# Optimization experiments

Measured on AMD Instinct MI355X. Metric: run time of the kernel, lower is better.

## Reference

```python
import jax, jax.numpy as jnp
import numpy as np

N, E, H = 20000, 320000, 5
IND, OUT = 64, 64
D2 = 2 * OUT          # 128
CAT = OUT + D2        # 192
BN_EPS = 1e-5


def _bn(x, g, b, m, v):
    # eval-mode BatchNorm1d
    return (x - m) * jax.lax.rsqrt(v + BN_EPS) * g + b


def _gcn(x, W, b, src, dst, n):
    # PyG GCNConv: add self-loops (already in src/dst), sym-normalized aggregation
    h = x @ W                                             # [N, C]
    deg = jax.ops.segment_sum(jnp.ones_like(dst, dtype=h.dtype), dst, num_segments=n)
    dinv = jnp.where(deg > 0, jax.lax.rsqrt(deg), 0.0)
    norm = dinv[src] * dinv[dst]                          # [E']
    out = jax.ops.segment_sum(h[src] * norm[:, None], dst, num_segments=n)
    return out + b


def _gat(x, W, att_src, att_dst, b, src, dst, n, heads, c):
    # PyG GATConv (concat=False): per-edge attention, segment softmax over dst
    hx = (x @ W).reshape(n, heads, c)                     # [N, H, C]
    a_s = jnp.einsum('nhc,hc->nh', hx, att_src)           # [N, H]
    a_d = jnp.einsum('nhc,hc->nh', hx, att_dst)
    e = jax.nn.leaky_relu(a_s[src] + a_d[dst], 0.2)       # [E', H]
    m = jax.ops.segment_max(e, dst, num_segments=n)       # every node has a self-loop
    w = jnp.exp(e - m[dst])
    den = jax.ops.segment_sum(w, dst, num_segments=n)
    alpha = w / den[dst]                                  # [E', H]
    out = jax.ops.segment_sum(hx[src] * alpha[:, :, None], dst, num_segments=n)  # [N,H,C]
    return out.mean(axis=1) + b


def setup_inputs() -> dict:
    key = jax.random.key(0)
    ks = iter(jax.random.split(key, 64))
    rn = lambda *s: jax.random.normal(next(ks), s, dtype=jnp.float32) * 0.05
    d = {}
    d['x_in'] = jax.random.normal(next(ks), (N, IND), dtype=jnp.float32)
    d['edge_index'] = jax.random.randint(next(ks), (2, E), 0, N, dtype=jnp.int64)
    # nn1: indim -> 2*indim -> outdim -> 2*outdim
    d['nn1_w1'], d['nn1_b1'] = rn(IND, 2 * IND), rn(2 * IND)
    d['nn1_w2'], d['nn1_b2'] = rn(2 * IND, OUT), rn(OUT)
    d['nn1_w3'], d['nn1_b3'] = rn(OUT, D2), rn(D2)
    # batchnorms (eval mode: gamma, beta, running mean/var)
    for name, dim in (('bn0', D2), ('bn1', D2), ('bn2', OUT)):
        d[name + '_g'] = rn(dim) + 1.0
        d[name + '_b'] = rn(dim)
        d[name + '_m'] = rn(dim)
        d[name + '_v'] = jax.random.uniform(next(ks), (dim,), jnp.float32, 0.5, 1.5)
    d['gcn1_w'], d['gcn1_b'] = rn(D2, D2), rn(D2)
    d['gat1_w'] = rn(D2, H * D2)
    d['gat1_as'], d['gat1_ad'], d['gat1_b'] = rn(H, D2), rn(H, D2), rn(D2)
    d['gcn2_w'], d['gcn2_b'] = rn(D2, OUT), rn(OUT)
    d['gat2_w'] = rn(OUT, H * OUT)
    d['gat2_as'], d['gat2_ad'], d['gat2_b'] = rn(H, OUT), rn(H, OUT), rn(OUT)
    # node_pred MLP: 192 -> 96 -> 48 -> 24 -> 1
    d['mlp_w1'], d['mlp_b1'] = rn(CAT, CAT // 2), rn(CAT // 2)
    d['mlp_w2'], d['mlp_b2'] = rn(CAT // 2, CAT // 4), rn(CAT // 4)
    d['mlp_w3'], d['mlp_b3'] = rn(CAT // 4, CAT // 8), rn(CAT // 8)
    d['mlp_w4'], d['mlp_b4'] = rn(CAT // 8, 1), rn(1)
    return d


def reference(x_in, edge_index,
              nn1_w1, nn1_b1, nn1_w2, nn1_b2, nn1_w3, nn1_b3,
              bn0_g, bn0_b, bn0_m, bn0_v,
              gcn1_w, gcn1_b, gat1_w, gat1_as, gat1_ad, gat1_b,
              gcn2_w, gcn2_b, gat2_w, gat2_as, gat2_ad, gat2_b,
              bn1_g, bn1_b, bn1_m, bn1_v,
              bn2_g, bn2_b, bn2_m, bn2_v,
              mlp_w1, mlp_b1, mlp_w2, mlp_b2, mlp_w3, mlp_b3, mlp_w4, mlp_b4):
    n = x_in.shape[0]
    loop = jnp.arange(n, dtype=edge_index.dtype)
    src = jnp.concatenate([edge_index[0], loop])   # self-loops (GCN & GAT defaults)
    dst = jnp.concatenate([edge_index[1], loop])

    sp = jax.nn.softplus
    x = sp(x_in @ nn1_w1 + nn1_b1)
    x = sp(x @ nn1_w2 + nn1_b2)
    x = x @ nn1_w3 + nn1_b3
    x = jax.nn.leaky_relu(_bn(x, bn0_g, bn0_b, bn0_m, bn0_v), 0.01)

    x1 = _gcn(x, gcn1_w, gcn1_b, src, dst, n)
    x1 = _gat(x1, gat1_w, gat1_as, gat1_ad, gat1_b, src, dst, n, H, D2)
    x1 = jax.nn.leaky_relu(_bn(x1, bn1_g, bn1_b, bn1_m, bn1_v), 0.01)
    skip1 = x + x1

    x2 = _gcn(skip1, gcn2_w, gcn2_b, src, dst, n)
    x2 = _gat(x2, gat2_w, gat2_as, gat2_ad, gat2_b, src, dst, n, H, OUT)
    x2 = jax.nn.leaky_relu(_bn(x2, bn2_g, bn2_b, bn2_m, bn2_v), 0.01)

    xf = jnp.concatenate([skip1, x2], axis=1)      # [N, 192]
    h = sp(xf @ mlp_w1 + mlp_b1)
    h = sp(h @ mlp_w2 + mlp_b2)
    h = sp(h @ mlp_w3 + mlp_b3)
    node_probs = jax.nn.sigmoid(h @ mlp_w4 + mlp_b4)   # [N, 1]
    return xf, node_probs
```

## Files before the change

kernel.cpp:

```cpp
#include <hip/hip_runtime.h>
#include <hip/hip_bf16.h>
#include <math.h>
#include <stdint.h>

typedef __hip_bfloat16 bf16;
typedef __hip_bfloat162 bf162;
typedef __attribute__((ext_vector_type(8))) short short8;
typedef __attribute__((ext_vector_type(4))) float f32x4;
#define HEADS 5

static inline long long cdivll(long long a, long long b){ return (a + b - 1) / b; }

__device__ __forceinline__ float b2f(bf16 v){ return __bfloat162float(v); }
__device__ __forceinline__ bf16 f2b(float v){ return __float2bfloat16(v); }
__device__ __forceinline__ short f2bs(float x){ bf16 b = __float2bfloat16(x); return *reinterpret_cast<short*>(&b); }
__device__ __forceinline__ float ldp(const void* p, long long i, int f32){
  return f32 ? ((const float*)p)[i] : b2f(((const bf16*)p)[i]);
}
__device__ __forceinline__ int eidx(const int* ei, long long i, int i64){
  return i64 ? ei[2 * i] : ei[i];
}
__device__ __forceinline__ float lrelu(float x, float a){ return x >= 0.f ? x : a * x; }
__device__ __forceinline__ float splus(float x){ return fmaxf(x, 0.f) + log1pf(expf(-fabsf(x))); }

__global__ void k_detect(const unsigned short* xh, const int* ei, int* flags){
  __shared__ int r0[256], r1[256];
  int t = threadIdx.x;
  int nan_cnt = 0;
  for (int i = t; i < 8192; i += 256){
    unsigned short u = xh[i];
    if (((u >> 7) & 0xFF) == 0xFF) nan_cnt++;
  }
  int odd_nz = 0;
  for (int i = 1 + 2 * t; i < 1024; i += 512) if (ei[i] != 0) odd_nz++;
  r0[t] = nan_cnt; r1[t] = odd_nz; __syncthreads();
  for (int o = 128; o > 0; o >>= 1){
    if (t < o){ r0[t] += r0[t + o]; r1[t] += r1[t + o]; }
    __syncthreads();
  }
  if (t == 0){
    flags[0] = (r0[0] > 0) ? 1 : 0;
    flags[1] = (r1[0] == 0) ? 1 : 0;
  }
}

__global__ void k_stampfill(bf16* out, long long n, float code){
  long long i = (long long)blockIdx.x * blockDim.x + threadIdx.x;
  if (i < n) out[i] = f2b(i == 0 ? code : 0.f);
}

__global__ void k_hist(const int* ei, int E, int N, int* counts, const int* flags){
  int i64 = flags[1];
  int e = blockIdx.x * blockDim.x + threadIdx.x;
  if (e >= E + N) return;
  int d = (e < E) ? eidx(ei, (long long)E + e, i64) : (e - E);
  atomicAdd(&counts[d], 1);
}
__global__ __launch_bounds__(1024) void k_scan(const int* counts, int* rowptr, int N){
  __shared__ int sums[1024];
  int t = threadIdx.x;
  int chunk = (N + 1023) / 1024;
  int start = t * chunk;
  int end = start + chunk; if (end > N) end = N;
  int s = 0;
  for (int i = start; i < end; ++i) s += counts[i];
  sums[t] = s; __syncthreads();
  for (int o = 1; o < 1024; o <<= 1){
    int v = (t >= o) ? sums[t - o] : 0;
    __syncthreads();
    sums[t] += v;
    __syncthreads();
  }
  int run = (t == 0) ? 0 : sums[t - 1];
  for (int i = start; i < end; ++i){ rowptr[i] = run; run += counts[i]; }
  if (t == 0) rowptr[N] = sums[1023];
}
__global__ void k_scatter(const int* ei, int E, int N, const int* rowptr, int* cursor,
                          unsigned short* colu, const int* flags){
  int i64 = flags[1];
  int e = blockIdx.x * blockDim.x + threadIdx.x;
  if (e >= E + N) return;
  int s, d;
  if (e < E){ s = eidx(ei, e, i64); d = eidx(ei, (long long)E + e, i64); }
  else { s = d = e - E; }
  int pos = rowptr[d] + atomicAdd(&cursor[d], 1);
  colu[pos] = (unsigned short)s;
}
__global__ void k_dinv(const int* rowptr, float* dinv, int N){
  int i = blockIdx.x * blockDim.x + threadIdx.x;
  if (i < N) dinv[i] = rsqrtf((float)(rowptr[i + 1] - rowptr[i]));
}

struct PackDesc { const void* W; int K, Kp, C, Cp, off, hk; };
struct PackArgs { PackDesc d[10]; int total; };
__global__ void k_packall(PackArgs P, bf16* WTA, int* cnt, int ncnt, const int* flags){
  int f32 = flags[0];
  int idx = blockIdx.x * blockDim.x + threadIdx.x;
  if (idx >= P.total){
    int z = idx - P.total;
    if (z < ncnt) cnt[z] = 0;
    return;
  }
  int base = 0;
#pragma unroll
  for (int s = 0; s < 10; ++s){
    int sz = P.d[s].Kp * P.d[s].Cp;
    if (idx < base + sz){
      int local = idx - base;
      int c = local / P.d[s].Kp;
      int k = local - c * P.d[s].Kp;
      float v;
      if (P.d[s].hk){
        int h = k / P.d[s].K;
        int kk = k - h * P.d[s].K;
        v = (c < P.d[s].C)
          ? ldp(P.d[s].W, (long long)kk * (P.d[s].hk * P.d[s].C) + h * P.d[s].C + c, f32) : 0.f;
      } else {
        v = (k < P.d[s].K && c < P.d[s].C)
          ? ldp(P.d[s].W, (long long)k * P.d[s].C + c, f32) : 0.f;
      }
      WTA[P.d[s].off + local] = f2b(v);
      return;
    }
    base += sz;
  }
}

__global__ void k_att_fold(const void* w1, const void* as1, const void* ad1,
                           const void* w2, const void* as2, const void* ad2,
                           bf16* wta, const int* flags){
  int f32 = flags[0];
  int idx = blockIdx.x * blockDim.x + threadIdx.x;
  if (idx < 8192){
    int c = idx >> 7, k = idx & 127;
    float v = 0.f;
    if (c < 10){
      int h = (c < 5) ? c : c - 5;
      const void* aw = (c < 5) ? as1 : ad1;
      for (int j = 0; j < 128; ++j)
        v = fmaf(ldp(w1, (long long)k * 640 + h * 128 + j, f32), ldp(aw, h * 128 + j, f32), v);
    }
    wta[186368 + idx] = f2b(v);
  } else if (idx < 12288){
    int l = idx - 8192;
    int c = l >> 6, k = l & 63;
    float v = 0.f;
    if (c < 10){
      int h = (c < 5) ? c : c - 5;
      const void* aw = (c < 5) ? as2 : ad2;
      for (int j = 0; j < 64; ++j)
        v = fmaf(ldp(w2, (long long)k * 320 + h * 64 + j, f32), ldp(aw, h * 64 + j, f32), v);
    }
    wta[194560 + l] = f2b(v);
  }
}

__global__ __launch_bounds__(256) void k_nn1f(
    const void* xin, const bf16* WTA,
    const void* b1, const void* b2, const void* b3,
    const void* g0, const void* bb0, const void* m0, const void* v0,
    float* X, bf16* hx, int N, const int* flags)
{
  __shared__ bf16 s1[4][16][136];
  __shared__ bf16 s2[4][16][72];
  int f32 = flags[0];
  int t = threadIdx.x, wave = t >> 6, lane = t & 63;
  int quad = lane >> 4, l15 = lane & 15;
  int mbase = blockIdx.x * 64 + wave * 16;
  int m = mbase + l15; if (m > N - 1) m = N - 1;

  f32x4 a1[8];
#pragma unroll
  for (int j = 0; j < 8; ++j) a1[j] = (f32x4){0.f, 0.f, 0.f, 0.f};
#pragma unroll
  for (int k0 = 0; k0 < 64; k0 += 32){
    int ka = k0 + quad * 8;
    short8 af;
    if (!f32){
      af = *(const short8*)((const bf16*)xin + (size_t)m * 64 + ka);
    } else {
      const float* p = (const float*)xin + (size_t)m * 64 + ka;
      float4 v0v = *(const float4*)p;
      float4 v1v = *(const float4*)(p + 4);
      af[0] = f2bs(v0v.x); af[1] = f2bs(v0v.y); af[2] = f2bs(v0v.z); af[3] = f2bs(v0v.w);
      af[4] = f2bs(v1v.x); af[5] = f2bs(v1v.y); af[6] = f2bs(v1v.z); af[7] = f2bs(v1v.w);
    }
#pragma unroll
    for (int j = 0; j < 8; ++j){
      short8 bvv = *(const short8*)(WTA + (size_t)(16 * j + l15) * 64 + ka);
      a1[j] = __builtin_amdgcn_mfma_f32_16x16x32_bf16(af, bvv, a1[j], 0, 0, 0);
    }
  }
#pragma unroll
  for (int j = 0; j < 8; ++j){
    int c = 16 * j + l15;
    float bi = ldp(b1, c, f32);
#pragma unroll
    for (int r = 0; r < 4; ++r)
      s1[wave][quad * 4 + r][c] = f2b(splus(a1[j][r] + bi));
  }
  __syncthreads();

  f32x4 a2[4];
#pragma unroll
  for (int j = 0; j < 4; ++j) a2[j] = (f32x4){0.f, 0.f, 0.f, 0.f};
#pragma unroll
  for (int k0 = 0; k0 < 128; k0 += 32){
    int ka = k0 + quad * 8;
    short8 af = *(const short8*)&s1[wave][l15][ka];
#pragma unroll
    for (int j = 0; j < 4; ++j){
      short8 bvv = *(const short8*)(WTA + 8192 + (size_t)(16 * j + l15) * 128 + ka);
      a2[j] = __builtin_amdgcn_mfma_f32_16x16x32_bf16(af, bvv, a2[j], 0, 0, 0);
    }
  }
#pragma unroll
  for (int j = 0; j < 4; ++j){
    int c = 16 * j + l15;
    float bi = ldp(b2, c, f32);
#pragma unroll
    for (int r = 0; r < 4; ++r)
      s2[wave][quad * 4 + r][c] = f2b(splus(a2[j][r] + bi));
  }
  __syncthreads();

  f32x4 a3[8];
#pragma unroll
  for (int j = 0; j < 8; ++j) a3[j] = (f32x4){0.f, 0.f, 0.f, 0.f};
#pragma unroll
  for (int k0 = 0; k0 < 64; k0 += 32){
    int ka = k0 + quad * 8;
    short8 af = *(const short8*)&s2[wave][l15][ka];
#pragma unroll
    for (int j = 0; j < 8; ++j){
      short8 bvv = *(const short8*)(WTA + 16384 + (size_t)(16 * j + l15) * 64 + ka);
      a3[j] = __builtin_amdgcn_mfma_f32_16x16x32_bf16(af, bvv, a3[j], 0, 0, 0);
    }
  }
#pragma unroll
  for (int j = 0; j < 8; ++j){
    int c = 16 * j + l15;
    float bi = ldp(b3, c, f32);
    float g = ldp(g0, c, f32), be = ldp(bb0, c, f32), mm = ldp(m0, c, f32);
    float iv = rsqrtf(ldp(v0, c, f32) + 1e-5f);
#pragma unroll
    for (int r = 0; r < 4; ++r){
      int n = mbase + quad * 4 + r;
      if (n >= N) continue;
      float y = a3[j][r] + bi;
      y = (y - mm) * iv * g + be;
      y = lrelu(y, 0.01f);
      X[(size_t)n * 128 + c] = y;
      s1[wave][quad * 4 + r][c] = f2b(y);
    }
  }
  __syncthreads();

  f32x4 a4[8];
#pragma unroll
  for (int j = 0; j < 8; ++j) a4[j] = (f32x4){0.f, 0.f, 0.f, 0.f};
#pragma unroll
  for (int k0 = 0; k0 < 128; k0 += 32){
    int ka = k0 + quad * 8;
    short8 af = *(const short8*)&s1[wave][l15][ka];
#pragma unroll
    for (int j = 0; j < 8; ++j){
      short8 bvv = *(const short8*)(WTA + 24576 + (size_t)(16 * j + l15) * 128 + ka);
      a4[j] = __builtin_amdgcn_mfma_f32_16x16x32_bf16(af, bvv, a4[j], 0, 0, 0);
    }
  }
#pragma unroll
  for (int j = 0; j < 8; ++j){
    int c = 16 * j + l15;
#pragma unroll
    for (int r = 0; r < 4; ++r){
      int n = mbase + quad * 4 + r;
      if (n < N) hx[(size_t)n * 128 + c] = f2b(a4[j][r]);
    }
  }
}

__global__ __launch_bounds__(256) void k_mlpf(
    const void* dout, const bf16* WTA,
    const void* b1, const void* b2, const void* b3,
    const void* w4, const void* b4, void* outfin, int N, const int* flags)
{
  __shared__ bf16 s1[4][16][104];
  __shared__ bf16 s2[4][16][72];
  int f32 = flags[0];
  int t = threadIdx.x, wave = t >> 6, lane = t & 63;
  int quad = lane >> 4, l15 = lane & 15;
  int mbase = blockIdx.x * 64 + wave * 16;
  int m = mbase + l15; if (m > N - 1) m = N - 1;

  f32x4 a1[6];
#pragma unroll
  for (int j = 0; j < 6; ++j) a1[j] = (f32x4){0.f, 0.f, 0.f, 0.f};
#pragma unroll
  for (int k0 = 0; k0 < 192; k0 += 32){
    int ka = k0 + quad * 8;
    short8 af;
    if (!f32){
      af = *(const short8*)((const bf16*)dout + (size_t)m * 192 + ka);
    } else {
      const float* p = (const float*)dout + (size_t)m * 192 + ka;
      float4 v0 = *(const float4*)p;
      float4 v1 = *(const float4*)(p + 4);
      af[0] = f2bs(v0.x); af[1] = f2bs(v0.y); af[2] = f2bs(v0.z); af[3] = f2bs(v0.w);
      af[4] = f2bs(v1.x); af[5] = f2bs(v1.y); af[6] = f2bs(v1.z); af[7] = f2bs(v1.w);
    }
#pragma unroll
    for (int j = 0; j < 6; ++j){
      short8 bvv = *(const short8*)(WTA + 151552 + (size_t)(16 * j + l15) * 192 + ka);
      a1[j] = __builtin_amdgcn_mfma_f32_16x16x32_bf16(af, bvv, a1[j], 0, 0, 0);
    }
  }
#pragma unroll
  for (int j = 0; j < 6; ++j){
    int c = 16 * j + l15;
    float bi = ldp(b1, c, f32);
#pragma unroll
    for (int r = 0; r < 4; ++r)
      s1[wave][quad * 4 + r][c] = f2b(splus(a1[j][r] + bi));
  }
  __syncthreads();

  f32x4 a2[3];
#pragma unroll
  for (int j = 0; j < 3; ++j) a2[j] = (f32x4){0.f, 0.f, 0.f, 0.f};
#pragma unroll
  for (int k0 = 0; k0 < 96; k0 += 32){
    int ka = k0 + quad * 8;
    short8 af = *(const short8*)&s1[wave][l15][ka];
#pragma unroll
    for (int j = 0; j < 3; ++j){
      short8 bvv = *(const short8*)(WTA + 176128 + (size_t)(16 * j + l15) * 96 + ka);
      a2[j] = __builtin_amdgcn_mfma_f32_16x16x32_bf16(af, bvv, a2[j], 0, 0, 0);
    }
  }
#pragma unroll
  for (int j = 0; j < 4; ++j){
    int c = 16 * j + l15;
    if (j < 3){
      float bi = ldp(b2, c, f32);
#pragma unroll
      for (int r = 0; r < 4; ++r)
        s2[wave][quad * 4 + r][c] = f2b(splus(a2[j][r] + bi));
    } else {
#pragma unroll
      for (int r = 0; r < 4; ++r)
        s2[wave][quad * 4 + r][c] = f2b(0.f);
    }
  }
  __syncthreads();

  f32x4 a3[2];
#pragma unroll
  for (int j = 0; j < 2; ++j) a3[j] = (f32x4){0.f, 0.f, 0.f, 0.f};
#pragma unroll
  for (int k0 = 0; k0 < 64; k0 += 32){
    int ka = k0 + quad * 8;
    short8 af = *(const short8*)&s2[wave][l15][ka];
#pragma unroll
    for (int j = 0; j < 2; ++j){
      short8 bvv = *(const short8*)(WTA + 182272 + (size_t)(16 * j + l15) * 64 + ka);
      a3[j] = __builtin_amdgcn_mfma_f32_16x16x32_bf16(af, bvv, a3[j], 0, 0, 0);
    }
  }
  float pr[4] = {0.f, 0.f, 0.f, 0.f};
#pragma unroll
  for (int j = 0; j < 2; ++j){
    int c = 16 * j + l15;
    float w = (c < 24) ? ldp(w4, c, f32) : 0.f;
    float bi = (c < 24) ? ldp(b3, c, f32) : 0.f;
#pragma unroll
    for (int r = 0; r < 4; ++r)
      pr[r] = fmaf(splus(a3[j][r] + bi), w, pr[r]);
  }
#pragma unroll
  for (int r = 0; r < 4; ++r){
#pragma unroll
    for (int o = 1; o < 16; o <<= 1) pr[r] += __shfl_xor(pr[r], o);
    int n = mbase + quad * 4 + r;
    if (l15 == 0 && n < N){
      float p = 1.f / (1.f + expf(-(pr[r] + ldp(b4, 0, f32))));
      long long oi = (long long)N * 192 + n;
      if (f32) ((float*)outfin)[oi] = p; else ((bf16*)outfin)[oi] = f2b(p);
    }
  }
}

__global__ __launch_bounds__(256) void k_gcn_csr(
    const int* rowptr, const unsigned short* colu, const bf16* h,
    const float* dinv, const void* bias, bf16* outb, int N, int C,
    const bf16* watt, float* asd, const int* flags)
{
  int f32 = flags[0];
  int wid = (blockIdx.x * 256 + threadIdx.x) >> 6;
  int lane = threadIdx.x & 63;
  if (wid >= N) return;
  int i0 = rowptr[wid], i1 = rowptr[wid + 1];
  float dr = dinv[wid];
  if (C == 128){
    int coff = lane << 1;
    float ax[4] = {0.f, 0.f, 0.f, 0.f}, ay[4] = {0.f, 0.f, 0.f, 0.f};
    int i = i0;
    for (; i + 3 < i1; i += 4){
      int s[4] = {colu[i], colu[i + 1], colu[i + 2], colu[i + 3]};
#pragma unroll
      for (int e = 0; e < 4; ++e){
        bf162 v = *(const bf162*)(h + (size_t)s[e] * 128 + coff);
        float f = dinv[s[e]];
        ax[e] = fmaf(f, b2f(v.x), ax[e]); ay[e] = fmaf(f, b2f(v.y), ay[e]);
      }
    }
    for (; i < i1; ++i){
      int s0 = colu[i];
      bf162 v = *(const bf162*)(h + (size_t)s0 * 128 + coff);
      float f = dinv[s0];
      ax[0] = fmaf(f, b2f(v.x), ax[0]); ay[0] = fmaf(f, b2f(v.y), ay[0]);
    }
    float sx = (ax[0] + ax[1]) + (ax[2] + ax[3]);
    float sy = (ay[0] + ay[1]) + (ay[2] + ay[3]);
    float vx = sx * dr + ldp(bias, coff, f32);
    float vy = sy * dr + ldp(bias, coff + 1, f32);
    bf162 o; o.x = f2b(vx); o.y = f2b(vy);
    *(bf162*)(outb + (size_t)wid * 128 + coff) = o;
    if (watt){
      float myv = 0.f;
#pragma unroll
      for (int hh = 0; hh < 10; ++hh){
        bf162 w = *(const bf162*)(watt + hh * 128 + coff);
        float p = vx * b2f(w.x) + vy * b2f(w.y);
#pragma unroll
        for (int o2 = 1; o2 < 64; o2 <<= 1) p += __shfl_xor(p, o2);
        if (lane == hh) myv = p;
      }
      if (lane < 10) asd[(size_t)wid * 10 + lane] = myv;
    }
  } else {
    int half = lane >> 5, hl = lane & 31;
    int coff = hl << 1;
    float ax = 0.f, ay = 0.f, bx = 0.f, by = 0.f;
    int i = i0;
    for (; i + 3 < i1; i += 4){
      int sA = colu[i + half], sB = colu[i + 2 + half];
      bf162 vA = *(const bf162*)(h + (size_t)sA * 64 + coff);
      bf162 vB = *(const bf162*)(h + (size_t)sB * 64 + coff);
      float fA = dinv[sA], fB = dinv[sB];
      ax = fmaf(fA, b2f(vA.x), ax); ay = fmaf(fA, b2f(vA.y), ay);
      bx = fmaf(fB, b2f(vB.x), bx); by = fmaf(fB, b2f(vB.y), by);
    }
    for (; i + 1 < i1; i += 2){
      int s = colu[i + half];
      bf162 v = *(const bf162*)(h + (size_t)s * 64 + coff);
      float f = dinv[s];
      ax = fmaf(f, b2f(v.x), ax); ay = fmaf(f, b2f(v.y), ay);
    }
    if (i < i1 && half == 0){
      int s = colu[i];
      bf162 v = *(const bf162*)(h + (size_t)s * 64 + coff);
      float f = dinv[s];
      ax = fmaf(f, b2f(v.x), ax); ay = fmaf(f, b2f(v.y), ay);
    }
    ax += bx; ay += by;
    ax += __shfl_xor(ax, 32);
    ay += __shfl_xor(ay, 32);
    float vx = ax * dr + ldp(bias, coff, f32);
    float vy = ay * dr + ldp(bias, coff + 1, f32);
    if (half == 0){
      bf162 o; o.x = f2b(vx); o.y = f2b(vy);
      *(bf162*)(outb + (size_t)wid * 64 + coff) = o;
    }
    if (watt){
      float myv = 0.f;
#pragma unroll
      for (int hh = 0; hh < 10; ++hh){
        bf162 w = *(const bf162*)(watt + hh * 64 + coff);
        float p = vx * b2f(w.x) + vy * b2f(w.y);
#pragma unroll
        for (int o2 = 1; o2 < 32; o2 <<= 1) p += __shfl_xor(p, o2);
        if (lane == hh) myv = p;
      }
      if (lane < 10) asd[(size_t)wid * 10 + lane] = myv;
    }
  }
}

template<int K>
__global__ __launch_bounds__(1024) void k_gat_proj(
    const int* rowptr, const unsigned short* colu, const bf16* bbx,
    const float* asd, const bf16* WT, const void* bias,
    const void* bg, const void* bbp, const void* bm, const void* bv,
    const float* skip, void* dout, int c2off,
    const bf16* WT2, bf16* hx, int N, const int* flags)
{
  constexpr int KP  = HEADS * K;
  constexpr int AGP = (K == 128) ? 648 : 328;
  constexpr int C   = K;
  constexpr int NCG = C / 16;
  constexpr int KSEG = KP / 2;
  __shared__ bf16 agg[16][AGP];
  __shared__ float als[16][HEADS][64];
  __shared__ unsigned short ssrc[16][64];
  int f32 = flags[0];
  int t = threadIdx.x, wave = t >> 6, lane = t & 63;
  int quad = lane >> 4, l15 = lane & 15;
  int rb = blockIdx.x * 16;

  int wid = rb + wave;
  if (wid < N){
    int i0 = rowptr[wid], i1 = rowptr[wid + 1];
    float adr[HEADS];
#pragma unroll
    for (int h = 0; h < HEADS; ++h) adr[h] = asd[(size_t)wid * 10 + 5 + h];
    float mx[HEADS];
#pragma unroll
    for (int h = 0; h < HEADS; ++h) mx[h] = -1e30f;
    for (int i = i0 + lane; i < i1; i += 64){
      int s = colu[i];
#pragma unroll
      for (int h = 0; h < HEADS; ++h){
        float e = lrelu(asd[(size_t)s * 10 + h] + adr[h], 0.2f);
        mx[h] = fmaxf(mx[h], e);
      }
    }
#pragma unroll
    for (int h = 0; h < HEADS; ++h)
      for (int o = 32; o > 0; o >>= 1) mx[h] = fmaxf(mx[h], __shfl_xor(mx[h], o));
    float den[HEADS];
#pragma unroll
    for (int h = 0; h < HEADS; ++h) den[h] = 0.f;
    for (int i = i0 + lane; i < i1; i += 64){
      int s = colu[i];
#pragma unroll
      for (int h = 0; h < HEADS; ++h){
        float e = lrelu(asd[(size_t)s * 10 + h] + adr[h], 0.2f);
        den[h] += expf(e - mx[h]);
      }
    }
#pragma unroll
    for (int h = 0; h < HEADS; ++h){
      for (int o = 32; o > 0; o >>= 1) den[h] += __shfl_xor(den[h], o);
      den[h] = 1.f / (den[h] * (float)HEADS);
    }
    if constexpr (K == 128){
      int coff = lane << 1;
      float ax[HEADS], ay[HEADS];
#pragma unroll
      for (int h = 0; h < HEADS; ++h){ ax[h] = 0.f; ay[h] = 0.f; }
      for (int base = i0; base < i1; base += 64){
        int iend = i1 - base; if (iend > 64) iend = 64;
        int i = base + lane;
        if (i < i1){
          int s = colu[i];
          ssrc[wave][lane] = (unsigned short)s;
#pragma unroll
          for (int h = 0; h < HEADS; ++h){
            float e = lrelu(asd[(size_t)s * 10 + h] + adr[h], 0.2f);
            als[wave][h][lane] = expf(e - mx[h]) * den[h];
          }
        }
        asm volatile("s_waitcnt lgkmcnt(0)" ::: "memory");
        int j = 0;
        for (; j + 3 < iend; j += 4){
          int s4[4];
#pragma unroll
          for (int e = 0; e < 4; ++e) s4[e] = ssrc[wave][j + e];
          bf162 v[4];
#pragma unroll
          for (int e = 0; e < 4; ++e) v[e] = *(const bf162*)(bbx + (size_t)s4[e] * 128 + coff);
#pragma unroll
          for (int e = 0; e < 4; ++e){
            float fx = b2f(v[e].x), fy = b2f(v[e].y);
#pragma unroll
            for (int h = 0; h < HEADS; ++h){
              float a = als[wave][h][j + e];
              ax[h] = fmaf(a, fx, ax[h]); ay[h] = fmaf(a, fy, ay[h]);
            }
          }
        }
        for (; j < iend; ++j){
          int s = ssrc[wave][j];
          bf162 v = *(const bf162*)(bbx + (size_t)s * 128 + coff);
          float fx = b2f(v.x), fy = b2f(v.y);
#pragma unroll
          for (int h = 0; h < HEADS; ++h){
            float a = als[wave][h][j];
            ax[h] = fmaf(a, fx, ax[h]); ay[h] = fmaf(a, fy, ay[h]);
          }
        }
      }
#pragma unroll
      for (int h = 0; h < HEADS; ++h){
        bf162 o; o.x = f2b(ax[h]); o.y = f2b(ay[h]);
        *(bf162*)&agg[wave][h * 128 + coff] = o;
      }
    } else {
      int half = lane >> 5, hl = lane & 31;
      int coff = hl << 1;
      float ax[HEADS], ay[HEADS];
#pragma unroll
      for (int h = 0; h < HEADS; ++h){ ax[h] = 0.f; ay[h] = 0.f; }
      for (int base = i0; base < i1; base += 64){
        int iend = i1 - base; if (iend > 64) iend = 64;
        int i = base + lane;
        if (i < i1){
          int s = colu[i];
          ssrc[wave][lane] = (unsigned short)s;
#pragma unroll
          for (int h = 0; h < HEADS; ++h){
            float e = lrelu(asd[(size_t)s * 10 + h] + adr[h], 0.2f);
            als[wave][h][lane] = expf(e - mx[h]) * den[h];
          }
        }
        asm volatile("s_waitcnt lgkmcnt(0)" ::: "memory");
        int j = 0;
        for (; j + 3 < iend; j += 4){
          int sA = ssrc[wave][j + half], sB = ssrc[wave][j + 2 + half];
          bf162 vA = *(const bf162*)(bbx + (size_t)sA * 64 + coff);
          bf162 vB = *(const bf162*)(bbx + (size_t)sB * 64 + coff);
          float Ax = b2f(vA.x), Ay = b2f(vA.y), Bx = b2f(vB.x), By = b2f(vB.y);
#pragma unroll
          for (int h = 0; h < HEADS; ++h){
            float aA = als[wave][h][j + half], aB = als[wave][h][j + 2 + half];
            ax[h] = fmaf(aA, Ax, ax[h]); ay[h] = fmaf(aA, Ay, ay[h]);
            ax[h] = fmaf(aB, Bx, ax[h]); ay[h] = fmaf(aB, By, ay[h]);
          }
        }
        for (; j + 1 < iend; j += 2){
          int s = ssrc[wave][j + half];
          bf162 v = *(const bf162*)(bbx + (size_t)s * 64 + coff);
          float fx = b2f(v.x), fy = b2f(v.y);
#pragma unroll
          for (int h = 0; h < HEADS; ++h){
            float a = als[wave][h][j + half];
            ax[h] = fmaf(a, fx, ax[h]); ay[h] = fmaf(a, fy, ay[h]);
          }
        }
        if (j < iend && half == 0){
          int s = ssrc[wave][j];
          bf162 v = *(const bf162*)(bbx + (size_t)s * 64 + coff);
          float fx = b2f(v.x), fy = b2f(v.y);
#pragma unroll
          for (int h = 0; h < HEADS; ++h){
            float a = als[wave][h][j];
            ax[h] = fmaf(a, fx, ax[h]); ay[h] = fmaf(a, fy, ay[h]);
          }
        }
      }
#pragma unroll
      for (int h = 0; h < HEADS; ++h){
        ax[h] += __shfl_xor(ax[h], 32);
        ay[h] += __shfl_xor(ay[h], 32);
      }
      if (half == 0){
#pragma unroll
        for (int h = 0; h < HEADS; ++h){
          bf162 o; o.x = f2b(ax[h]); o.y = f2b(ay[h]);
          *(bf162*)&agg[wave][h * 64 + coff] = o;
        }
      }
    }
  }
  __syncthreads();

  auto red = reinterpret_cast<float(*)[16][20]>(&als[0][0][0]);
  int cg = wave & (NCG - 1);
  int kh = wave / NCG;
  f32x4 acc = (f32x4){0.f, 0.f, 0.f, 0.f};
  if (kh < 2){
#pragma unroll
    for (int ks = 0; ks < KSEG; ks += 32){
      int ka = kh * KSEG + ks + quad * 8;
      short8 af = *(const short8*)&agg[l15][ka];
      short8 bvv = *(const short8*)(WT + (size_t)(cg * 16 + l15) * KP + ka);
      acc = __builtin_amdgcn_mfma_f32_16x16x32_bf16(af, bvv, acc, 0, 0, 0);
    }
  }
  if (kh == 1){
#pragma unroll
    for (int r = 0; r < 4; ++r)
      red[cg][quad * 4 + r][l15] = acc[r];
  }
  __syncthreads();
  if (kh == 0){
#pragma unroll
    for (int r = 0; r < 4; ++r)
      acc[r] += red[cg][quad * 4 + r][l15];
    int c = cg * 16 + l15;
    float bi = ldp(bias, c, f32);
    float g = ldp(bg, c, f32), be = ldp(bbp, c, f32), mm = ldp(bm, c, f32);
    float iv = rsqrtf(ldp(bv, c, f32) + 1e-5f);
#pragma unroll
    for (int r = 0; r < 4; ++r){
      int n = rb + quad * 4 + r;
      if (n >= N) continue;
      float y = acc[r] + bi;
      y = (y - mm) * iv * g + be;
      y = lrelu(y, 0.01f);
      if (skip) y += skip[(size_t)n * 128 + c];
      size_t o = (size_t)n * 192 + c2off + c;
      if (f32) ((float*)dout)[o] = y; else ((bf16*)dout)[o] = f2b(y);
      if (WT2) agg[quad * 4 + r][c] = f2b(y);
    }
  }

  if constexpr (K == 128){
    if (WT2){
      __syncthreads();
      int cg2 = wave & 3, kh2 = wave >> 2;
      f32x4 a2 = (f32x4){0.f, 0.f, 0.f, 0.f};
      int ka = kh2 * 32 + quad * 8;
      short8 af = *(const short8*)&agg[l15][ka];
      short8 bvv = *(const short8*)(WT2 + (size_t)(cg2 * 16 + l15) * 128 + ka);
      a2 = __builtin_amdgcn_mfma_f32_16x16x32_bf16(af, bvv, a2, 0, 0, 0);
      auto red2 = reinterpret_cast<float(*)[16][20]>(&als[0][0][0]);
      if (kh2 > 0){
        int slot = (kh2 - 1) * 4 + cg2;
#pragma unroll
        for (int r = 0; r < 4; ++r)
          red2[slot][quad * 4 + r][l15] = a2[r];
      }
      __syncthreads();
      if (kh2 == 0){
#pragma unroll
        for (int s = 0; s < 3; ++s)
#pragma unroll
          for (int r = 0; r < 4; ++r)
            a2[r] += red2[s * 4 + cg2][quad * 4 + r][l15];
        int c2 = cg2 * 16 + l15;
#pragma unroll
        for (int r = 0; r < 4; ++r){
          int n = rb + quad * 4 + r;
          if (n < N) hx[(size_t)n * 64 + c2] = f2b(a2[r]);
        }
      }
    }
  }
}

extern "C" void kernel_launch(void* const* d_in, const int* in_sizes, int n_in,
                              void* d_out, int out_size, void* d_ws, size_t ws_size,
                              hipStream_t stream)
{
  const void* x_in   = d_in[0];
  const int*  ei     = (const int*)d_in[1];
  const void *nn1_w1 = d_in[2], *nn1_b1 = d_in[3], *nn1_w2 = d_in[4], *nn1_b2 = d_in[5];
  const void *nn1_w3 = d_in[6], *nn1_b3 = d_in[7];
  const void *bn0_g = d_in[8],  *bn0_b = d_in[9],  *bn0_m = d_in[10], *bn0_v = d_in[11];
  const void *bn1_g = d_in[12], *bn1_b = d_in[13], *bn1_m = d_in[14], *bn1_v = d_in[15];
  const void *bn2_g = d_in[16], *bn2_b = d_in[17], *bn2_m = d_in[18], *bn2_v = d_in[19];
  const void *gcn1_w = d_in[20], *gcn1_b = d_in[21];
  const void *gat1_w = d_in[22], *gat1_as = d_in[23], *gat1_ad = d_in[24], *gat1_b = d_in[25];
  const void *gcn2_w = d_in[26], *gcn2_b = d_in[27];
  const void *gat2_w = d_in[28], *gat2_as = d_in[29], *gat2_ad = d_in[30], *gat2_b = d_in[31];
  const void *mlp_w1 = d_in[32], *mlp_b1 = d_in[33], *mlp_w2 = d_in[34], *mlp_b2 = d_in[35];
  const void *mlp_w3 = d_in[36], *mlp_b3 = d_in[37], *mlp_w4 = d_in[38], *mlp_b4 = d_in[39];
  (void)n_in;

  const int N  = in_sizes[0] / 64;
  const int E  = in_sizes[1] / 2;
  const int Ep = E + N;
  const int TB = 256;

  if ((long long)out_size != (long long)N * 193 || N > 65535){
    k_stampfill<<<(int)cdivll(out_size, TB), TB, 0, stream>>>((bf16*)d_out, out_size, 8192.f);
    return;
  }
  size_t need = 2900ull * (size_t)N + 500000ull;
  if (ws_size < need){
    k_stampfill<<<(int)cdivll(out_size, TB), TB, 0, stream>>>((bf16*)d_out, out_size, 1024.f);
    return;
  }

  char* wsb = (char*)d_ws;
  int*   FLAGS = (int*)wsb;
  float* X    = (float*)(wsb + 16);
  float* A    = X + (size_t)N * 128;
  float* B    = A + (size_t)N * 128;
  float* DINV = B + (size_t)N * 128;
  float* AS   = DINV + N;
  int*   ROWP = (int*)(AS + (size_t)N * 2 * HEADS);
  unsigned short* COLU = (unsigned short*)(ROWP + N + 1);
  bf16*  HX   = (bf16*)(COLU + ((Ep + 7) & ~7));
  bf16*  WTA  = (bf16*)(((uintptr_t)(HX + (size_t)N * 640) + 15) & ~(uintptr_t)15);
  bf16*  BB   = (bf16*)A;
  int* CNT = (int*)AS;
  int* CUR = CNT + N;
  const int ATT1_OFF = 186368;
  const int ATT2_OFF = 194560;

  k_detect<<<1, 256, 0, stream>>>((const unsigned short*)x_in, ei, FLAGS);

  PackArgs P;
  P.d[0] = {nn1_w1,  64, 64, 128, 128, 0, 0};
  P.d[1] = {nn1_w2, 128,128,  64,  64, 8192, 0};
  P.d[2] = {nn1_w3,  64, 64, 128, 128, 16384, 0};
  P.d[3] = {gcn1_w, 128,128, 128, 128, 24576, 0};
  P.d[4] = {gat1_w, 128,640, 128, 128, 40960, 5};
  P.d[5] = {gcn2_w, 128,128,  64,  64, 122880, 0};
  P.d[6] = {gat2_w,  64,320,  64,  64, 131072, 5};
  P.d[7] = {mlp_w1, 192,192,  96, 128, 151552, 0};
  P.d[8] = {mlp_w2,  96, 96,  48,  64, 176128, 0};
  P.d[9] = {mlp_w3,  48, 64,  24,  64, 182272, 0};
  P.total = 186368;
  k_packall<<<(int)cdivll(P.total + 2 * N, TB), TB, 0, stream>>>(P, WTA, CNT, 2 * N, FLAGS);
  k_att_fold<<<48, 256, 0, stream>>>(gat1_w, gat1_as, gat1_ad, gat2_w, gat2_as, gat2_ad, WTA, FLAGS);

  k_hist<<<(int)cdivll(Ep, TB), TB, 0, stream>>>(ei, E, N, CNT, FLAGS);
  k_scan<<<1, 1024, 0, stream>>>(CNT, ROWP, N);
  k_scatter<<<(int)cdivll(Ep, TB), TB, 0, stream>>>(ei, E, N, ROWP, CUR, COLU, FLAGS);
  k_dinv<<<(int)cdivll(N, TB), TB, 0, stream>>>(ROWP, DINV, N);

  int rowsg = (int)cdivll(N, 4);
  int rowsf = (int)cdivll(N, 64);
  int rows16 = (int)cdivll(N, 16);

  k_nn1f<<<rowsf, 256, 0, stream>>>(x_in, WTA, nn1_b1, nn1_b2, nn1_b3,
                                    bn0_g, bn0_b, bn0_m, bn0_v, X, HX, N, FLAGS);

  k_gcn_csr<<<rowsg, 256, 0, stream>>>(ROWP, COLU, HX, DINV, gcn1_b, BB, N, 128,
                                       WTA + ATT1_OFF, AS, FLAGS);

  k_gat_proj<128><<<rows16, 1024, 0, stream>>>(ROWP, COLU, BB, AS, WTA + 40960, gat1_b,
      bn1_g, bn1_b, bn1_m, bn1_v, X, d_out, 0, WTA + 122880, HX, N, FLAGS);

  k_gcn_csr<<<rowsg, 256, 0, stream>>>(ROWP, COLU, HX, DINV, gcn2_b, BB, N, 64,
                                       WTA + ATT2_OFF, AS, FLAGS);

  k_gat_proj<64><<<rows16, 1024, 0, stream>>>(ROWP, COLU, BB, AS, WTA + 131072, gat2_b,
      bn2_g, bn2_b, bn2_m, bn2_v, nullptr, d_out, 128, nullptr, nullptr, N, FLAGS);

  k_mlpf<<<rowsf, 256, 0, stream>>>(d_out, WTA, mlp_b1, mlp_b2, mlp_b3,
                                    mlp_w4, mlp_b4, d_out, N, FLAGS);
}
```

Measured before the change: 455.7 us.

## Fuse GAT softmax into single pass with deferred normalization and wider unroll

Removes the separate max and denominator passes over each node's edges in the fused GAT aggregate kernel. Attention weights are now computed as unshifted exp (clamped at 80) in the same pass that gathers features, with the per-head denominators summed alongside and applied once at the end. The gather loop is also unrolled to 8 edges to keep more loads in flight. This saves two rounds of index and attention-score reads per node, but drops the max-subtraction for numerical safety, relying on the clamp and small score magnitudes.

```diff
diff --git a/kernel.cpp b/kernel.cpp
--- a/kernel.cpp
+++ b/kernel.cpp
@@ -514,36 +514,10 @@
     float adr[HEADS];
 #pragma unroll
     for (int h = 0; h < HEADS; ++h) adr[h] = asd[(size_t)wid * 10 + 5 + h];
-    float mx[HEADS];
-#pragma unroll
-    for (int h = 0; h < HEADS; ++h) mx[h] = -1e30f;
-    for (int i = i0 + lane; i < i1; i += 64){
-      int s = colu[i];
-#pragma unroll
-      for (int h = 0; h < HEADS; ++h){
-        float e = lrelu(asd[(size_t)s * 10 + h] + adr[h], 0.2f);
-        mx[h] = fmaxf(mx[h], e);
-      }
-    }
-#pragma unroll
-    for (int h = 0; h < HEADS; ++h)
-      for (int o = 32; o > 0; o >>= 1) mx[h] = fmaxf(mx[h], __shfl_xor(mx[h], o));
-    float den[HEADS];
-#pragma unroll
-    for (int h = 0; h < HEADS; ++h) den[h] = 0.f;
-    for (int i = i0 + lane; i < i1; i += 64){
-      int s = colu[i];
-#pragma unroll
-      for (int h = 0; h < HEADS; ++h){
-        float e = lrelu(asd[(size_t)s * 10 + h] + adr[h], 0.2f);
-        den[h] += expf(e - mx[h]);
-      }
-    }
-#pragma unroll
-    for (int h = 0; h < HEADS; ++h){
-      for (int o = 32; o > 0; o >>= 1) den[h] += __shfl_xor(den[h], o);
-      den[h] = 1.f / (den[h] * (float)HEADS);
-    }
+    float denl[HEADS];
+#pragma unroll
+    for (int h = 0; h < HEADS; ++h) denl[h] = 0.f;
+
     if constexpr (K == 128){
       int coff = lane << 1;
       float ax[HEADS], ay[HEADS];
@@ -554,24 +528,31 @@
         int i = base + lane;
         if (i < i1){
           int s = colu[i];
+          float2 q0 = *(const float2*)(asd + (size_t)s * 10);
+          float2 q1 = *(const float2*)(asd + (size_t)s * 10 + 2);
+          float q4 = asd[(size_t)s * 10 + 4];
+          float w0 = expf(fminf(lrelu(q0.x + adr[0], 0.2f), 80.f));
+          float w1 = expf(fminf(lrelu(q0.y + adr[1], 0.2f), 80.f));
+          float w2 = expf(fminf(lrelu(q1.x + adr[2], 0.2f), 80.f));
+          float w3 = expf(fminf(lrelu(q1.y + adr[3], 0.2f), 80.f));
+          float w4 = expf(fminf(lrelu(q4 + adr[4], 0.2f), 80.f));
           ssrc[wave][lane] = (unsigned short)s;
-#pragma unroll
-          for (int h = 0; h < HEADS; ++h){
-            float e = lrelu(asd[(size_t)s * 10 + h] + adr[h], 0.2f);
-            als[wave][h][lane] = expf(e - mx[h]) * den[h];
-          }
+          als[wave][0][lane] = w0; als[wave][1][lane] = w1;
+          als[wave][2][lane] = w2; als[wave][3][lane] = w3;
+          als[wave][4][lane] = w4;
+          denl[0] += w0; denl[1] += w1; denl[2] += w2; denl[3] += w3; denl[4] += w4;
         }
         asm volatile("s_waitcnt lgkmcnt(0)" ::: "memory");
         int j = 0;
-        for (; j + 3 < iend; j += 4){
-          int s4[4];
-#pragma unroll
-          for (int e = 0; e < 4; ++e) s4[e] = ssrc[wave][j + e];
-          bf162 v[4];
-#pragma unroll
-          for (int e = 0; e < 4; ++e) v[e] = *(const bf162*)(bbx + (size_t)s4[e] * 128 + coff);
-#pragma unroll
-          for (int e = 0; e < 4; ++e){
+        for (; j + 7 < iend; j += 8){
+          int s8[8];
+#pragma unroll
+          for (int e = 0; e < 8; ++e) s8[e] = ssrc[wave][j + e];
+          bf162 v[8];
+#pragma unroll
+          for (int e = 0; e < 8; ++e) v[e] = *(const bf162*)(bbx + (size_t)s8[e] * 128 + coff);
+#pragma unroll
+          for (int e = 0; e < 8; ++e){
             float fx = b2f(v[e].x), fy = b2f(v[e].y);
 #pragma unroll
             for (int h = 0; h < HEADS; ++h){
@@ -580,6 +561,23 @@
             }
           }
         }
+        for (; j + 3 < iend; j += 4){
+          int s4[4];
+#pragma unroll
+          for (int e = 0; e < 4; ++e) s4[e] = ssrc[wave][j + e];
+          bf162 v[4];
+#pragma unroll
+          for (int e = 0; e < 4; ++e) v[e] = *(const bf162*)(bbx + (size_t)s4[e] * 128 + coff);
+#pragma unroll
+          for (int e = 0; e < 4; ++e){
+            float fx = b2f(v[e].x), fy = b2f(v[e].y);
+#pragma unroll
+            for (int h = 0; h < HEADS; ++h){
+              float a = als[wave][h][j + e];
+              ax[h] = fmaf(a, fx, ax[h]); ay[h] = fmaf(a, fy, ay[h]);
+            }
+          }
+        }
         for (; j < iend; ++j){
           int s = ssrc[wave][j];
           bf162 v = *(const bf162*)(bbx + (size_t)s * 128 + coff);
@@ -591,9 +589,16 @@
           }
         }
       }
+      float dnv[HEADS];
 #pragma unroll
       for (int h = 0; h < HEADS; ++h){
-        bf162 o; o.x = f2b(ax[h]); o.y = f2b(ay[h]);
+        float d = denl[h];
+        for (int o = 32; o > 0; o >>= 1) d += __shfl_xor(d, o);
+        dnv[h] = 1.f / (d * (float)HEADS);
+      }
+#pragma unroll
+      for (int h = 0; h < HEADS; ++h){
+        bf162 o; o.x = f2b(ax[h] * dnv[h]); o.y = f2b(ay[h] * dnv[h]);
         *(bf162*)&agg[wave][h * 128 + coff] = o;
       }
     } else {
@@ -607,15 +612,41 @@
         int i = base + lane;
         if (i < i1){
           int s = colu[i];
+          float2 q0 = *(const float2*)(asd + (size_t)s * 10);
+          float2 q1 = *(const float2*)(asd + (size_t)s * 10 + 2);
+          float q4 = asd[(size_t)s * 10 + 4];
+          float w0 = expf(fminf(lrelu(q0.x + adr[0], 0.2f), 80.f));
+          float w1 = expf(fminf(lrelu(q0.y + adr[1], 0.2f), 80.f));
+          float w2 = expf(fminf(lrelu(q1.x + adr[2], 0.2f), 80.f));
+          float w3 = expf(fminf(lrelu(q1.y + adr[3], 0.2f), 80.f));
+          float w4 = expf(fminf(lrelu(q4 + adr[4], 0.2f), 80.f));
           ssrc[wave][lane] = (unsigned short)s;
-#pragma unroll
-          for (int h = 0; h < HEADS; ++h){
-            float e = lrelu(asd[(size_t)s * 10 + h] + adr[h], 0.2f);
-            als[wave][h][lane] = expf(e - mx[h]) * den[h];
-          }
+          als[wave][0][lane] = w0; als[wave][1][lane] = w1;
+          als[wave][2][lane] = w2; als[wave][3][lane] = w3;
+          als[wave][4][lane] = w4;
+          denl[0] += w0; denl[1] += w1; denl[2] += w2; denl[3] += w3; denl[4] += w4;
         }
         asm volatile("s_waitcnt lgkmcnt(0)" ::: "memory");
         int j = 0;
+        for (; j + 7 < iend; j += 8){
+          int sA = ssrc[wave][j + half],     sB = ssrc[wave][j + 2 + half];
+          int sC = ssrc[wave][j + 4 + half], sD = ssrc[wave][j + 6 + half];
+          bf162 vA = *(const bf162*)(bbx + (size_t)sA * 64 + coff);
+          bf162 vB = *(const bf162*)(bbx + (size_t)sB * 64 + coff);
+          bf162 vC = *(const bf162*)(bbx + (size_t)sC * 64 + coff);
+          bf162 vD = *(const bf162*)(bbx + (size_t)sD * 64 + coff);
+          float Ax = b2f(vA.x), Ay = b2f(vA.y), Bx = b2f(vB.x), By = b2f(vB.y);
+          float Cx = b2f(vC.x), Cy = b2f(vC.y), Dx = b2f(vD.x), Dy = b2f(vD.y);
+#pragma unroll
+          for (int h = 0; h < HEADS; ++h){
+            float aA = als[wave][h][j + half],     aB = als[wave][h][j + 2 + half];
+            float aC = als[wave][h][j + 4 + half], aD = als[wave][h][j + 6 + half];
+            ax[h] = fmaf(aA, Ax, ax[h]); ay[h] = fmaf(aA, Ay, ay[h]);
+            ax[h] = fmaf(aB, Bx, ax[h]); ay[h] = fmaf(aB, By, ay[h]);
+            ax[h] = fmaf(aC, Cx, ax[h]); ay[h] = fmaf(aC, Cy, ay[h]);
+            ax[h] = fmaf(aD, Dx, ax[h]); ay[h] = fmaf(aD, Dy, ay[h]);
+          }
+        }
         for (; j + 3 < iend; j += 4){
           int sA = ssrc[wave][j + half], sB = ssrc[wave][j + 2 + half];
           bf162 vA = *(const bf162*)(bbx + (size_t)sA * 64 + coff);
@@ -649,6 +680,13 @@
           }
         }
       }
+      float dnv[HEADS];
+#pragma unroll
+      for (int h = 0; h < HEADS; ++h){
+        float d = denl[h];
+        for (int o = 32; o > 0; o >>= 1) d += __shfl_xor(d, o);
+        dnv[h] = 1.f / (d * (float)HEADS);
+      }
 #pragma unroll
       for (int h = 0; h < HEADS; ++h){
         ax[h] += __shfl_xor(ax[h], 32);
@@ -657,7 +695,7 @@
       if (half == 0){
 #pragma unroll
         for (int h = 0; h < HEADS; ++h){
-          bf162 o; o.x = f2b(ax[h]); o.y = f2b(ay[h]);
+          bf162 o; o.x = f2b(ax[h] * dnv[h]); o.y = f2b(ay[h] * dnv[h]);
           *(bf162*)&agg[wave][h * 64 + coff] = o;
         }
       }
```

New measurement: 517.3 us. 1.14x slower.
